# Performance work log

Hardware: AMD Instinct MI355X
Metric: run time of the kernel (lower is better)

## Reference

```python
import jax, jax.numpy as jnp
import numpy as np

N = 500000   # total objects across all segments
B = 8192     # number of segments (batch)
OBJ = 64     # object_size
H = 128      # hidden_size
CTX = 256    # context_size


def setup_inputs() -> dict:
    key = jax.random.key(0)
    ks = jax.random.split(key, 9)
    s = 0.05
    x = jax.random.normal(ks[0], (N, OBJ), jnp.float32)
    context = jax.random.normal(ks[1], (B, CTX), jnp.float32)
    # sorted segment ids, every segment nonempty (ragged lengths collapse to ~N/B each)
    segment_ids = (jnp.arange(N, dtype=jnp.int32) * B) // N
    W0 = jax.random.normal(ks[2], (OBJ, H), jnp.float32) * s
    b0 = jnp.zeros((H,), jnp.float32)
    W1 = jax.random.normal(ks[3], (H, H), jnp.float32) * s
    b1 = jnp.zeros((H,), jnp.float32)
    Wkv = jax.random.normal(ks[4], (H, 2 * H), jnp.float32) * s
    bkv = jnp.zeros((2 * H,), jnp.float32)
    Wq = jax.random.normal(ks[5], (CTX, H), jnp.float32) * s
    bq = jnp.zeros((H,), jnp.float32)
    gain = jnp.full((1, 1), -0.5 * np.log(H), jnp.float32)
    return dict(x=x, context=context, segment_ids=segment_ids,
                W0=W0, b0=b0, W1=W1, b1=b1, Wkv=Wkv, bkv=bkv,
                Wq=Wq, bq=bq, gain=gain)


def reference(x, context, segment_ids, W0, b0, W1, b1, Wkv, bkv, Wq, bq, gain):
    h = jax.nn.relu(x @ W0 + b0)          # [N, H]
    h = jax.nn.relu(h @ W1 + b1)          # [N, H]
    kv = h @ Wkv + bkv                    # [N, 2H]
    hsz = Wkv.shape[1] // 2
    key_, value = kv[:, :hsz], kv[:, hsz:]
    q = context @ Wq + bq                 # [B, H]
    qg = q[segment_ids]                   # gather == repeat_interleave
    logits = jnp.exp(gain)[0, 0] * jnp.sum(key_ * qg, axis=1)  # [N]
    # per-segment stable softmax
    m = jax.ops.segment_max(logits, segment_ids, num_segments=B)
    z = jnp.exp(logits - m[segment_ids])
    denom = jax.ops.segment_sum(z, segment_ids, num_segments=B)
    w = z / denom[segment_ids]            # [N]
    # per-segment softmax-weighted sum of values -> [B, H]
    embedding = jax.ops.segment_sum(w[:, None] * value, segment_ids, num_segments=B)
    return embedding, w[:, None]
```

## Files before the change

### kernel.cpp

```cpp
#include <hip/hip_runtime.h>
#include <math.h>

#define NN   500000
#define BB   8192
#define OBJ  64
#define HH   128
#define CTXD 256

typedef __attribute__((ext_vector_type(8))) short short8;
typedef __attribute__((ext_vector_type(4))) float f32x4;

#define W0HI  0
#define W0LO  8192
#define W1HI  16384
#define W1LO  32768
#define PG_OFF  4292608
#define CQ_OFF  8486912
#define WS_NEED 8519680

__device__ __forceinline__ unsigned short f2bf(float f) {
    unsigned int u = __float_as_uint(f);
    u += 0x7FFFu + ((u >> 16) & 1u);
    return (unsigned short)(u >> 16);
}
__device__ __forceinline__ float bf2f(unsigned short h) {
    return __uint_as_float(((unsigned int)h) << 16);
}
__device__ __forceinline__ void split2(float v, unsigned short& hi, unsigned short& lo) {
    unsigned int u = __float_as_uint(v);
    hi = (unsigned short)(u >> 16);
    lo = f2bf(v - bf2f(hi));
}

__global__ void prep_frags(const float* __restrict__ W0,
                           const float* __restrict__ W1,
                           unsigned short* __restrict__ wsb)
{
    const int t = blockIdx.x * 256 + threadIdx.x;
    if (t >= 48 * 64) return;
    const int f = t >> 6, lane = t & 63;
    const float* W; int KS, bhi, blo, fl;
    if (f < 16) { W = W0; KS = 2; bhi = W0HI; blo = W0LO; fl = f; }
    else        { W = W1; KS = 4; bhi = W1HI; blo = W1LO; fl = f - 16; }
    const int nt = fl / KS, ks = fl - nt * KS;
    const int n  = nt * 16 + (lane & 15);
    const int k0 = ks * 32 + (lane >> 4) * 8;
    short8 h8, l8;
    #pragma unroll
    for (int j = 0; j < 8; ++j) {
        float v = W[(size_t)(k0 + j) * HH + n];
        unsigned short h, l; split2(v, h, l);
        h8[j] = (short)h; l8[j] = (short)l;
    }
    const int off = fl * 512 + lane * 8;
    *(short8*)(wsb + bhi + off) = h8;
    *(short8*)(wsb + blo + off) = l8;
}

__global__ void qp_gemm(const float* __restrict__ context,
                        const float* __restrict__ Wq,
                        const float* __restrict__ bq,
                        const float* __restrict__ Wkv,
                        const float* __restrict__ bkv,
                        float* __restrict__ pg, float* __restrict__ cq)
{
    __shared__ float ctxs[16 * CTXD];
    __shared__ float qs[16 * HH];
    const int tid = threadIdx.x;
    const int seg0 = blockIdx.x * 16;
    {
        const float4* cg = (const float4*)(context + (size_t)seg0 * CTXD);
        float4* cs = (float4*)ctxs;
        for (int i = tid; i < 16 * CTXD / 4; i += 128) cs[i] = cg[i];
    }
    __syncthreads();
    {
        float acc[16];
        const float bqv = bq[tid];
        #pragma unroll
        for (int s = 0; s < 16; ++s) acc[s] = bqv;
        #pragma unroll 4
        for (int k = 0; k < CTXD; ++k) {
            const float wv = Wq[(size_t)k * HH + tid];
            #pragma unroll
            for (int s = 0; s < 16; ++s) acc[s] = fmaf(ctxs[s * CTXD + k], wv, acc[s]);
        }
        #pragma unroll
        for (int s = 0; s < 16; ++s) qs[s * HH + tid] = acc[s];
    }
    __syncthreads();
    {
        float acc[16];
        #pragma unroll
        for (int s = 0; s < 16; ++s) acc[s] = 0.f;
        for (int c = 0; c < HH; c += 4) {
            const float4 wk = *(const float4*)(Wkv + (size_t)tid * 2 * HH + c);
            #pragma unroll
            for (int s = 0; s < 16; ++s) {
                float a = acc[s];
                a = fmaf(wk.x, qs[s * HH + c + 0], a);
                a = fmaf(wk.y, qs[s * HH + c + 1], a);
                a = fmaf(wk.z, qs[s * HH + c + 2], a);
                a = fmaf(wk.w, qs[s * HH + c + 3], a);
                acc[s] = a;
            }
        }
        #pragma unroll
        for (int s = 0; s < 16; ++s) pg[(size_t)(seg0 + s) * HH + tid] = acc[s];
    }
    if (tid < 16) {
        float a = 0.f;
        for (int c = 0; c < HH; ++c) a = fmaf(bkv[c], qs[tid * HH + c], a);
        cq[seg0 + tid] = a;
    }
}

__launch_bounds__(256, 4)
__global__ void seg_wave(const float* __restrict__ x,
                         const float* __restrict__ context,
                         const float* __restrict__ Wq,   const float* __restrict__ bq,
                         const float* __restrict__ Wkv,  const float* __restrict__ bkv,
                         const float* __restrict__ b0,
                         const float* __restrict__ b1,
                         const float* __restrict__ gain,
                         const unsigned short* __restrict__ wsb,
                         const float* __restrict__ pg,
                         const float* __restrict__ cq,
                         float* __restrict__ out_emb, float* __restrict__ out_w)
{
    __shared__ unsigned short h0f[2][4][4][512];
    __shared__ __align__(16) float psum[64][4];
    __shared__ float uu[HH];
    __shared__ float qv[HH];

    const int tid  = threadIdx.x;
    const int w    = tid >> 6;
    const int lane = tid & 63;
    const int seg  = blockIdx.x;
    const int nl = lane & 15, qq = lane >> 4;

    const int start = (int)(((long long)seg * NN + BB - 1) / BB);
    const int end   = (int)(((long long)(seg + 1) * NN + BB - 1) / BB);
    const int count = end - start;

    if (!pg) {
        if (tid < HH) {
            float a = bq[tid];
            for (int k = 0; k < CTXD; ++k)
                a = fmaf(context[(size_t)seg * CTXD + k], Wq[(size_t)k * HH + tid], a);
            qv[tid] = a;
        }
        __syncthreads();
    }

    f32x4 a1acc[2][4];
    #pragma unroll
    for (int t = 0; t < 2; ++t)
        #pragma unroll
        for (int mt = 0; mt < 4; ++mt) a1acc[t][mt] = {0.f, 0.f, 0.f, 0.f};

    #pragma unroll
    for (int ks = 0; ks < 2; ++ks) {
        short8 axh[4], axl[4];
        #pragma unroll
        for (int mt = 0; mt < 4; ++mt) {
            int row = start + mt * 16 + nl;
            if (row > NN - 1) row = NN - 1;
            const float* xp = x + (size_t)row * OBJ + ks * 32 + qq * 8;
            const float4 a0 = *(const float4*)xp;
            const float4 a1 = *(const float4*)(xp + 4);
            const float vv[8] = {a0.x, a0.y, a0.z, a0.w, a1.x, a1.y, a1.z, a1.w};
            #pragma unroll
            for (int j = 0; j < 8; ++j) {
                unsigned short h, l; split2(vv[j], h, l);
                axh[mt][j] = (short)h; axl[mt][j] = (short)l;
            }
        }
        #pragma unroll
        for (int t = 0; t < 2; ++t) {
            const int fb = ((2 * w + t) * 2 + ks) * 512 + lane * 8;
            const short8 bh = *(const short8*)(wsb + W0HI + fb);
            const short8 bl = *(const short8*)(wsb + W0LO + fb);
            #pragma unroll
            for (int mt = 0; mt < 4; ++mt) {
                a1acc[t][mt] = __builtin_amdgcn_mfma_f32_16x16x32_bf16(axh[mt], bh, a1acc[t][mt], 0, 0, 0);
                a1acc[t][mt] = __builtin_amdgcn_mfma_f32_16x16x32_bf16(axh[mt], bl, a1acc[t][mt], 0, 0, 0);
                a1acc[t][mt] = __builtin_amdgcn_mfma_f32_16x16x32_bf16(axl[mt], bh, a1acc[t][mt], 0, 0, 0);
            }
        }
    }

    #pragma unroll
    for (int t = 0; t < 2; ++t) {
        const float bb = b0[w * 32 + t * 16 + nl];
        #pragma unroll
        for (int mt = 0; mt < 4; ++mt) {
            #pragma unroll
            for (int r = 0; r < 4; ++r) {
                float hv = fmaxf(a1acc[t][mt][r] + bb, 0.f);
                unsigned short h, l; split2(hv, h, l);
                const int idx = ((qq * 4 + r) + 32 * t + 16 * (nl >> 3)) * 8 + (nl & 7);
                h0f[0][w][mt][idx] = h;
                h0f[1][w][mt][idx] = l;
            }
        }
    }
    __syncthreads();

    f32x4 acc2[2][4];
    #pragma unroll
    for (int t = 0; t < 2; ++t)
        #pragma unroll
        for (int mt = 0; mt < 4; ++mt) acc2[t][mt] = {0.f, 0.f, 0.f, 0.f};

    #pragma unroll
    for (int j = 0; j < 4; ++j) {
        short8 ah[4], al[4];
        #pragma unroll
        for (int mt = 0; mt < 4; ++mt) {
            ah[mt] = *(const short8*)&h0f[0][j][mt][lane * 8];
            al[mt] = *(const short8*)&h0f[1][j][mt][lane * 8];
        }
        #pragma unroll
        for (int t = 0; t < 2; ++t) {
            const int fb = ((2 * w + t) * 4 + j) * 512 + lane * 8;
            const short8 bh = *(const short8*)(wsb + W1HI + fb);
            const short8 bl = *(const short8*)(wsb + W1LO + fb);
            #pragma unroll
            for (int mt = 0; mt < 4; ++mt) {
                acc2[t][mt] = __builtin_amdgcn_mfma_f32_16x16x32_bf16(ah[mt], bh, acc2[t][mt], 0, 0, 0);
                acc2[t][mt] = __builtin_amdgcn_mfma_f32_16x16x32_bf16(ah[mt], bl, acc2[t][mt], 0, 0, 0);
                acc2[t][mt] = __builtin_amdgcn_mfma_f32_16x16x32_bf16(al[mt], bh, acc2[t][mt], 0, 0, 0);
            }
        }
    }

    #pragma unroll
    for (int t = 0; t < 2; ++t) {
        const float b1v = b1[(2 * w + t) * 16 + nl];
        #pragma unroll
        for (int mt = 0; mt < 4; ++mt)
            #pragma unroll
            for (int r = 0; r < 4; ++r)
                acc2[t][mt][r] = fmaxf(acc2[t][mt][r] + b1v, 0.f);
    }

    float pv[2], cqv;
    if (pg) {
        #pragma unroll
        for (int t = 0; t < 2; ++t) pv[t] = pg[(size_t)seg * HH + (2 * w + t) * 16 + nl];
        cqv = cq[seg];
    } else {
        cqv = 0.f;
        for (int c = 0; c < HH; ++c) cqv = fmaf(bkv[c], qv[c], cqv);
        #pragma unroll
        for (int t = 0; t < 2; ++t) {
            const int k = (2 * w + t) * 16 + nl;
            float s = 0.f;
            for (int c = 0; c < HH; ++c) s = fmaf(Wkv[(size_t)k * 2 * HH + c], qv[c], s);
            pv[t] = s;
        }
    }

    #pragma unroll
    for (int mt = 0; mt < 4; ++mt) {
        #pragma unroll
        for (int r = 0; r < 4; ++r) {
            float s = acc2[0][mt][r] * pv[0] + acc2[1][mt][r] * pv[1];
            #pragma unroll
            for (int off = 1; off <= 8; off <<= 1) s += __shfl_xor(s, off, 64);
            if (nl == 0) psum[mt * 16 + qq * 4 + r][w] = s;
        }
    }
    __syncthreads();

    const float eg = expf(gain[0]);
    float lp[4][4];
    #pragma unroll
    for (int mt = 0; mt < 4; ++mt) {
        #pragma unroll
        for (int r = 0; r < 4; ++r) {
            const int row = mt * 16 + qq * 4 + r;
            const float4 ps = *(const float4*)psum[row];
            lp[mt][r] = (row < count) ? eg * (ps.x + ps.y + ps.z + ps.w + cqv) : -INFINITY;
        }
    }

    float m = lp[0][0];
    #pragma unroll
    for (int mt = 0; mt < 4; ++mt)
        #pragma unroll
        for (int r = 0; r < 4; ++r) m = fmaxf(m, lp[mt][r]);
    m = fmaxf(m, __shfl_xor(m, 16, 64));
    m = fmaxf(m, __shfl_xor(m, 32, 64));
    float wv[4][4], Z = 0.f;
    #pragma unroll
    for (int mt = 0; mt < 4; ++mt)
        #pragma unroll
        for (int r = 0; r < 4; ++r) { wv[mt][r] = expf(lp[mt][r] - m); Z += wv[mt][r]; }
    Z += __shfl_xor(Z, 16, 64);
    Z += __shfl_xor(Z, 32, 64);
    const float rZ = 1.f / Z;
    #pragma unroll
    for (int mt = 0; mt < 4; ++mt)
        #pragma unroll
        for (int r = 0; r < 4; ++r) wv[mt][r] *= rZ;
    if (w == 0 && nl == 0) {
        #pragma unroll
        for (int mt = 0; mt < 4; ++mt)
            #pragma unroll
            for (int r = 0; r < 4; ++r) {
                const int row = mt * 16 + qq * 4 + r;
                if (row < count) out_w[start + row] = wv[mt][r];
            }
    }

    #pragma unroll
    for (int t = 0; t < 2; ++t) {
        float s = 0.f;
        #pragma unroll
        for (int mt = 0; mt < 4; ++mt)
            #pragma unroll
            for (int r = 0; r < 4; ++r) s = fmaf(wv[mt][r], acc2[t][mt][r], s);
        s += __shfl_xor(s, 16, 64);
        s += __shfl_xor(s, 32, 64);
        if (qq == 0) uu[(2 * w + t) * 16 + nl] = s;
    }
    __syncthreads();

    float* esum = &psum[0][0];
    {
        const int c = tid & 127, kh = tid >> 7;
        float e = (kh == 0) ? bkv[HH + c] : 0.f;
        #pragma unroll 4
        for (int k = kh * 64; k < kh * 64 + 64; ++k)
            e = fmaf(uu[k], Wkv[(size_t)k * 2 * HH + HH + c], e);
        esum[tid] = e;
    }
    __syncthreads();
    if (tid < HH)
        out_emb[(size_t)seg * HH + tid] = esum[tid] + esum[tid + HH];
}

extern "C" void kernel_launch(void* const* d_in, const int* in_sizes, int n_in,
                              void* d_out, int out_size, void* d_ws, size_t ws_size,
                              hipStream_t stream)
{
    (void)in_sizes; (void)n_in; (void)out_size;
    const float* x    = (const float*)d_in[0];
    const float* ctx  = (const float*)d_in[1];
    const float* W0   = (const float*)d_in[3];
    const float* b0   = (const float*)d_in[4];
    const float* W1   = (const float*)d_in[5];
    const float* b1   = (const float*)d_in[6];
    const float* Wkv  = (const float*)d_in[7];
    const float* bkv  = (const float*)d_in[8];
    const float* Wq   = (const float*)d_in[9];
    const float* bq   = (const float*)d_in[10];
    const float* gain = (const float*)d_in[11];

    float* out_emb = (float*)d_out;
    float* out_w   = (float*)d_out + (size_t)BB * HH;

    unsigned short* wsb = (unsigned short*)d_ws;
    const bool big_ws = (ws_size >= (size_t)WS_NEED);
    float* pg = big_ws ? (float*)((char*)d_ws + PG_OFF) : nullptr;
    float* cq = big_ws ? (float*)((char*)d_ws + CQ_OFF) : nullptr;

    hipLaunchKernelGGL(prep_frags, dim3(12), dim3(256), 0, stream, W0, W1, wsb);
    if (big_ws) {
        hipLaunchKernelGGL(qp_gemm, dim3(BB / 16), dim3(128), 0, stream,
                           ctx, Wq, bq, Wkv, bkv, pg, cq);
    }
    hipLaunchKernelGGL(seg_wave, dim3(BB), dim3(256), 0, stream,
                       x, ctx, Wq, bq, Wkv, bkv, b0, b1, gain, wsb, pg, cq,
                       out_emb, out_w);
}
```

Baseline: 392.3 us.

## Split segment work across eight waves with LDS-staged input fragments

Each segment block grows from 256 to 512 threads, so every wave owns one 16-column output tile instead of two. The x rows are loaded once, split into bf16 hi/lo pairs and staged through shared memory, rather than each wave reloading and splitting all rows itself. Logit partial sums and the final value projection are reduced across eight waves. This halves per-wave register state and removes redundant global x loads. In exchange it adds extra barriers and LDS traffic, and the launch bound now asks for 8 blocks of 512 threads per CU.

```diff
diff --git a/kernel.cpp b/kernel.cpp
--- a/kernel.cpp
+++ b/kernel.cpp
@@ -115,7 +115,7 @@
     }
 }
 
-__launch_bounds__(256, 4)
+__launch_bounds__(512, 8)
 __global__ void seg_wave(const float* __restrict__ x,
                          const float* __restrict__ context,
                          const float* __restrict__ Wq,   const float* __restrict__ bq,
@@ -128,8 +128,8 @@
                          const float* __restrict__ cq,
                          float* __restrict__ out_emb, float* __restrict__ out_w)
 {
-    __shared__ unsigned short h0f[2][4][4][512];
-    __shared__ __align__(16) float psum[64][4];
+    __shared__ unsigned short h0f[2 * 4 * 4 * 512];
+    __shared__ __align__(16) float psum[64][8];
     __shared__ float uu[HH];
     __shared__ float qv[HH];
 
@@ -153,120 +153,117 @@
         __syncthreads();
     }
 
-    f32x4 a1acc[2][4];
-    #pragma unroll
-    for (int t = 0; t < 2; ++t)
-        #pragma unroll
-        for (int mt = 0; mt < 4; ++mt) a1acc[t][mt] = {0.f, 0.f, 0.f, 0.f};
-
+    {
+        const int ks = w >> 2, mt = w & 3;
+        int row = start + mt * 16 + nl;
+        if (row > NN - 1) row = NN - 1;
+        const float* xp = x + (size_t)row * OBJ + ks * 32 + qq * 8;
+        const float4 a0 = *(const float4*)xp;
+        const float4 a1 = *(const float4*)(xp + 4);
+        const float vv[8] = {a0.x, a0.y, a0.z, a0.w, a1.x, a1.y, a1.z, a1.w};
+        short8 h8, l8;
+        #pragma unroll
+        for (int j = 0; j < 8; ++j) {
+            unsigned short h, l; split2(vv[j], h, l);
+            h8[j] = (short)h; l8[j] = (short)l;
+        }
+        *(short8*)&h0f[((0 * 2 + ks) * 4 + mt) * 512 + lane * 8] = h8;
+        *(short8*)&h0f[((1 * 2 + ks) * 4 + mt) * 512 + lane * 8] = l8;
+    }
+    const float eg = expf(gain[0]);
+    __syncthreads();
+
+    f32x4 a1acc[4];
+    #pragma unroll
+    for (int mt = 0; mt < 4; ++mt) a1acc[mt] = {0.f, 0.f, 0.f, 0.f};
     #pragma unroll
     for (int ks = 0; ks < 2; ++ks) {
-        short8 axh[4], axl[4];
-        #pragma unroll
-        for (int mt = 0; mt < 4; ++mt) {
-            int row = start + mt * 16 + nl;
-            if (row > NN - 1) row = NN - 1;
-            const float* xp = x + (size_t)row * OBJ + ks * 32 + qq * 8;
-            const float4 a0 = *(const float4*)xp;
-            const float4 a1 = *(const float4*)(xp + 4);
-            const float vv[8] = {a0.x, a0.y, a0.z, a0.w, a1.x, a1.y, a1.z, a1.w};
-            #pragma unroll
-            for (int j = 0; j < 8; ++j) {
-                unsigned short h, l; split2(vv[j], h, l);
-                axh[mt][j] = (short)h; axl[mt][j] = (short)l;
+        const int fb = (w * 2 + ks) * 512 + lane * 8;
+        const short8 bh = *(const short8*)(wsb + W0HI + fb);
+        const short8 bl = *(const short8*)(wsb + W0LO + fb);
+        short8 ah[4], al[4];
+        #pragma unroll
+        for (int mt = 0; mt < 4; ++mt) {
+            ah[mt] = *(const short8*)&h0f[((0 * 2 + ks) * 4 + mt) * 512 + lane * 8];
+            al[mt] = *(const short8*)&h0f[((1 * 2 + ks) * 4 + mt) * 512 + lane * 8];
+        }
+        #pragma unroll
+        for (int mt = 0; mt < 4; ++mt) {
+            a1acc[mt] = __builtin_amdgcn_mfma_f32_16x16x32_bf16(ah[mt], bh, a1acc[mt], 0, 0, 0);
+            a1acc[mt] = __builtin_amdgcn_mfma_f32_16x16x32_bf16(ah[mt], bl, a1acc[mt], 0, 0, 0);
+            a1acc[mt] = __builtin_amdgcn_mfma_f32_16x16x32_bf16(al[mt], bh, a1acc[mt], 0, 0, 0);
+        }
+    }
+    __syncthreads();
+
+    {
+        const float bb = b0[w * 16 + nl];
+        const int j = w >> 1;
+        const int kqh = (w & 1) * 2 + (nl >> 3);
+        const int e = nl & 7;
+        #pragma unroll
+        for (int mt = 0; mt < 4; ++mt) {
+            #pragma unroll
+            for (int r = 0; r < 4; ++r) {
+                float hv = fmaxf(a1acc[mt][r] + bb, 0.f);
+                unsigned short h, l; split2(hv, h, l);
+                const int idx = (qq * 4 + r + 16 * kqh) * 8 + e;
+                h0f[((0 * 4 + j) * 4 + mt) * 512 + idx] = h;
+                h0f[((1 * 4 + j) * 4 + mt) * 512 + idx] = l;
             }
         }
-        #pragma unroll
-        for (int t = 0; t < 2; ++t) {
-            const int fb = ((2 * w + t) * 2 + ks) * 512 + lane * 8;
-            const short8 bh = *(const short8*)(wsb + W0HI + fb);
-            const short8 bl = *(const short8*)(wsb + W0LO + fb);
-            #pragma unroll
-            for (int mt = 0; mt < 4; ++mt) {
-                a1acc[t][mt] = __builtin_amdgcn_mfma_f32_16x16x32_bf16(axh[mt], bh, a1acc[t][mt], 0, 0, 0);
-                a1acc[t][mt] = __builtin_amdgcn_mfma_f32_16x16x32_bf16(axh[mt], bl, a1acc[t][mt], 0, 0, 0);
-                a1acc[t][mt] = __builtin_amdgcn_mfma_f32_16x16x32_bf16(axl[mt], bh, a1acc[t][mt], 0, 0, 0);
-            }
-        }
-    }
-
-    #pragma unroll
-    for (int t = 0; t < 2; ++t) {
-        const float bb = b0[w * 32 + t * 16 + nl];
-        #pragma unroll
-        for (int mt = 0; mt < 4; ++mt) {
-            #pragma unroll
-            for (int r = 0; r < 4; ++r) {
-                float hv = fmaxf(a1acc[t][mt][r] + bb, 0.f);
-                unsigned short h, l; split2(hv, h, l);
-                const int idx = ((qq * 4 + r) + 32 * t + 16 * (nl >> 3)) * 8 + (nl & 7);
-                h0f[0][w][mt][idx] = h;
-                h0f[1][w][mt][idx] = l;
-            }
-        }
-    }
-    __syncthreads();
-
-    f32x4 acc2[2][4];
-    #pragma unroll
-    for (int t = 0; t < 2; ++t)
-        #pragma unroll
-        for (int mt = 0; mt < 4; ++mt) acc2[t][mt] = {0.f, 0.f, 0.f, 0.f};
-
-    #pragma unroll
-    for (int j = 0; j < 4; ++j) {
-        short8 ah[4], al[4];
-        #pragma unroll
-        for (int mt = 0; mt < 4; ++mt) {
-            ah[mt] = *(const short8*)&h0f[0][j][mt][lane * 8];
-            al[mt] = *(const short8*)&h0f[1][j][mt][lane * 8];
-        }
-        #pragma unroll
-        for (int t = 0; t < 2; ++t) {
-            const int fb = ((2 * w + t) * 4 + j) * 512 + lane * 8;
-            const short8 bh = *(const short8*)(wsb + W1HI + fb);
-            const short8 bl = *(const short8*)(wsb + W1LO + fb);
-            #pragma unroll
-            for (int mt = 0; mt < 4; ++mt) {
-                acc2[t][mt] = __builtin_amdgcn_mfma_f32_16x16x32_bf16(ah[mt], bh, acc2[t][mt], 0, 0, 0);
-                acc2[t][mt] = __builtin_amdgcn_mfma_f32_16x16x32_bf16(ah[mt], bl, acc2[t][mt], 0, 0, 0);
-                acc2[t][mt] = __builtin_amdgcn_mfma_f32_16x16x32_bf16(al[mt], bh, acc2[t][mt], 0, 0, 0);
-            }
-        }
-    }
-
-    #pragma unroll
-    for (int t = 0; t < 2; ++t) {
-        const float b1v = b1[(2 * w + t) * 16 + nl];
-        #pragma unroll
-        for (int mt = 0; mt < 4; ++mt)
-            #pragma unroll
-            for (int r = 0; r < 4; ++r)
-                acc2[t][mt][r] = fmaxf(acc2[t][mt][r] + b1v, 0.f);
-    }
-
-    float pv[2], cqv;
+    }
+    __syncthreads();
+
+    float pv, cqv;
     if (pg) {
-        #pragma unroll
-        for (int t = 0; t < 2; ++t) pv[t] = pg[(size_t)seg * HH + (2 * w + t) * 16 + nl];
+        pv = pg[(size_t)seg * HH + w * 16 + nl];
         cqv = cq[seg];
     } else {
         cqv = 0.f;
         for (int c = 0; c < HH; ++c) cqv = fmaf(bkv[c], qv[c], cqv);
-        #pragma unroll
-        for (int t = 0; t < 2; ++t) {
-            const int k = (2 * w + t) * 16 + nl;
-            float s = 0.f;
-            for (int c = 0; c < HH; ++c) s = fmaf(Wkv[(size_t)k * 2 * HH + c], qv[c], s);
-            pv[t] = s;
-        }
+        const int k = w * 16 + nl;
+        float s = 0.f;
+        for (int c = 0; c < HH; ++c) s = fmaf(Wkv[(size_t)k * 2 * HH + c], qv[c], s);
+        pv = s;
+    }
+
+    f32x4 acc2[4];
+    #pragma unroll
+    for (int mt = 0; mt < 4; ++mt) acc2[mt] = {0.f, 0.f, 0.f, 0.f};
+    #pragma unroll
+    for (int j = 0; j < 4; ++j) {
+        short8 ah[4], al[4];
+        #pragma unroll
+        for (int mt = 0; mt < 4; ++mt) {
+            ah[mt] = *(const short8*)&h0f[((0 * 4 + j) * 4 + mt) * 512 + lane * 8];
+            al[mt] = *(const short8*)&h0f[((1 * 4 + j) * 4 + mt) * 512 + lane * 8];
+        }
+        const int fb = (w * 4 + j) * 512 + lane * 8;
+        const short8 bh = *(const short8*)(wsb + W1HI + fb);
+        const short8 bl = *(const short8*)(wsb + W1LO + fb);
+        #pragma unroll
+        for (int mt = 0; mt < 4; ++mt) {
+            acc2[mt] = __builtin_amdgcn_mfma_f32_16x16x32_bf16(ah[mt], bh, acc2[mt], 0, 0, 0);
+            acc2[mt] = __builtin_amdgcn_mfma_f32_16x16x32_bf16(ah[mt], bl, acc2[mt], 0, 0, 0);
+            acc2[mt] = __builtin_amdgcn_mfma_f32_16x16x32_bf16(al[mt], bh, acc2[mt], 0, 0, 0);
+        }
+    }
+
+    {
+        const float b1v = b1[w * 16 + nl];
+        #pragma unroll
+        for (int mt = 0; mt < 4; ++mt)
+            #pragma unroll
+            for (int r = 0; r < 4; ++r)
+                acc2[mt][r] = fmaxf(acc2[mt][r] + b1v, 0.f);
     }
 
     #pragma unroll
     for (int mt = 0; mt < 4; ++mt) {
         #pragma unroll
         for (int r = 0; r < 4; ++r) {
-            float s = acc2[0][mt][r] * pv[0] + acc2[1][mt][r] * pv[1];
+            float s = acc2[mt][r] * pv;
             #pragma unroll
             for (int off = 1; off <= 8; off <<= 1) s += __shfl_xor(s, off, 64);
             if (nl == 0) psum[mt * 16 + qq * 4 + r][w] = s;
@@ -274,15 +271,16 @@
     }
     __syncthreads();
 
-    const float eg = expf(gain[0]);
     float lp[4][4];
     #pragma unroll
     for (int mt = 0; mt < 4; ++mt) {
         #pragma unroll
         for (int r = 0; r < 4; ++r) {
             const int row = mt * 16 + qq * 4 + r;
-            const float4 ps = *(const float4*)psum[row];
-            lp[mt][r] = (row < count) ? eg * (ps.x + ps.y + ps.z + ps.w + cqv) : -INFINITY;
+            const float4 p0 = *(const float4*)&psum[row][0];
+            const float4 p1 = *(const float4*)&psum[row][4];
+            const float s8 = (p0.x + p0.y + p0.z + p0.w) + (p1.x + p1.y + p1.z + p1.w);
+            lp[mt][r] = (row < count) ? eg * (s8 + cqv) : -INFINITY;
         }
     }
 
@@ -315,16 +313,15 @@
             }
     }
 
-    #pragma unroll
-    for (int t = 0; t < 2; ++t) {
+    {
         float s = 0.f;
         #pragma unroll
         for (int mt = 0; mt < 4; ++mt)
             #pragma unroll
-            for (int r = 0; r < 4; ++r) s = fmaf(wv[mt][r], acc2[t][mt][r], s);
+            for (int r = 0; r < 4; ++r) s = fmaf(wv[mt][r], acc2[mt][r], s);
         s += __shfl_xor(s, 16, 64);
         s += __shfl_xor(s, 32, 64);
-        if (qq == 0) uu[(2 * w + t) * 16 + nl] = s;
+        if (qq == 0) uu[w * 16 + nl] = s;
     }
     __syncthreads();
 
@@ -333,13 +330,14 @@
         const int c = tid & 127, kh = tid >> 7;
         float e = (kh == 0) ? bkv[HH + c] : 0.f;
         #pragma unroll 4
-        for (int k = kh * 64; k < kh * 64 + 64; ++k)
+        for (int k = kh * 32; k < kh * 32 + 32; ++k)
             e = fmaf(uu[k], Wkv[(size_t)k * 2 * HH + HH + c], e);
         esum[tid] = e;
     }
     __syncthreads();
     if (tid < HH)
-        out_emb[(size_t)seg * HH + tid] = esum[tid] + esum[tid + HH];
+        out_emb[(size_t)seg * HH + tid] =
+            esum[tid] + esum[tid + 128] + esum[tid + 256] + esum[tid + 384];
 }
 
 extern "C" void kernel_launch(void* const* d_in, const int* in_sizes, int n_in,
@@ -372,7 +370,7 @@
         hipLaunchKernelGGL(qp_gemm, dim3(BB / 16), dim3(128), 0, stream,
                            ctx, Wq, bq, Wkv, bkv, pg, cq);
     }
-    hipLaunchKernelGGL(seg_wave, dim3(BB), dim3(256), 0, stream,
+    hipLaunchKernelGGL(seg_wave, dim3(BB), dim3(512), 0, stream,
                        x, ctx, Wq, bq, Wkv, bkv, b0, b1, gain, wsb, pg, cq,
                        out_emb, out_w);
 }
```

New measurement: 366.5 us. 6.6% less time.
